# Kernel optimization log

Hardware: AMD Instinct MI355X
Metric: run time of the kernel (lower is better)

The kernel has to match this reference:

```python
import jax, jax.numpy as jnp
import numpy as np

NUM_WIRES = 18
NUM_LAYERS = 3
BATCH = 64
DIM = 2 ** NUM_WIRES


def _apply_ry(psi, theta, w):
    # RY(t) = [[cos(t/2), -sin(t/2)], [sin(t/2), cos(t/2)]] on wire w (wire 0 = MSB)
    B = psi.shape[0]
    c = jnp.cos(theta * 0.5).astype(psi.dtype)
    s = jnp.sin(theta * 0.5).astype(psi.dtype)
    p = psi.reshape(B, 2 ** w, 2, -1)
    a, b = p[:, :, 0], p[:, :, 1]
    return jnp.stack([c * a - s * b, s * a + c * b], axis=2).reshape(B, -1)


def _apply_rz(psi, theta, w):
    # RZ(t) = diag(e^{-i t/2}, e^{+i t/2}) on wire w
    B = psi.shape[0]
    half = (theta * 0.5).astype(jnp.complex64)
    p0 = jnp.exp(-1j * half)
    p1 = jnp.exp(1j * half)
    p = psi.reshape(B, 2 ** w, 2, -1)
    return jnp.stack([p0 * p[:, :, 0], p1 * p[:, :, 1]], axis=2).reshape(B, -1)


def _apply_cnot_adjacent(psi, w):
    # CNOT with control w, target w+1: flip target bit where control bit = 1
    B = psi.shape[0]
    p = psi.reshape(B, 2 ** w, 2, 2, -1)
    p = p.at[:, :, 1].set(p[:, :, 1, ::-1])
    return p.reshape(B, -1)


def _expval_z(psi, w):
    # <Z_w> = P(bit_w = 0) - P(bit_w = 1)
    B = psi.shape[0]
    prob = (psi.real ** 2 + psi.imag ** 2).reshape(B, 2 ** w, 2, -1)
    p = prob.sum(axis=(1, 3))  # (B, 2)
    return p[:, 0] - p[:, 1]


def _circuit(psi, params):
    for layer in range(params.shape[0]):
        for w in range(NUM_WIRES):
            psi = _apply_ry(psi, params[layer, 0, w], w)
            psi = _apply_rz(psi, params[layer, 1, w], w)
        for w in range(NUM_WIRES - 1):
            psi = _apply_cnot_adjacent(psi, w)
    # expvals of PauliZ on every wire -> (B, num_wires)
    return jnp.stack([_expval_z(psi, w) for w in range(NUM_WIRES)], axis=-1)


def setup_inputs() -> dict:
    key = jax.random.key(0)
    k1, k2, k3, k4, k5 = jax.random.split(key, 5)
    state_re = jax.random.normal(k1, (BATCH, DIM), dtype=jnp.float32)
    state_im = jax.random.normal(k2, (BATCH, DIM), dtype=jnp.float32)
    norm = jnp.sqrt(jnp.sum(state_re ** 2 + state_im ** 2, axis=-1, keepdims=True))
    state_re = state_re / norm
    state_im = state_im / norm
    params = jax.random.normal(k3, (NUM_LAYERS, 2, NUM_WIRES), dtype=jnp.float32)
    head_w = jax.random.normal(k4, (1, NUM_WIRES), dtype=jnp.float32) / np.sqrt(NUM_WIRES)
    head_b = jax.random.normal(k5, (1,), dtype=jnp.float32) / np.sqrt(NUM_WIRES)
    return {"state_re": state_re, "state_im": state_im, "params": params,
            "head_w": head_w, "head_b": head_b}


def reference(state_re, state_im, params, head_w, head_b):
    psi = (state_re + 1j * state_im).astype(jnp.complex64)  # (B, 2^n)
    feats = _circuit(psi, params)                            # (B, n)
    out = feats @ head_w.T + head_b                          # (B, 1)
    return out[:, 0]
```

## Files before the change

### kernel.cpp

```cpp
#include <hip/hip_runtime.h>


#define LROW 36u
#define LDSW 2304u

static __device__ __forceinline__ float rfl(float x) {
    return __int_as_float(__builtin_amdgcn_readfirstlane(__float_as_int(x)));
}

static __device__ __forceinline__ void unpack2(unsigned u, float& re, float& im) {
    re = __uint_as_float(u << 16);
    im = __uint_as_float(u & 0xFFFF0000u);
}
static __device__ __forceinline__ unsigned packbf(float a, float b) {
    unsigned ua = __float_as_uint(a); ua += 0x7FFFu + ((ua >> 16) & 1u);
    unsigned ub = __float_as_uint(b); ub += 0x7FFFu + ((ub >> 16) & 1u);
    return (ua >> 16) | (ub & 0xFFFF0000u);
}

static __device__ __forceinline__ void sq_pair(float& a0r, float& a0i, float& a1r, float& a1i,
                                               float c, float s, float pc, float ps) {
    const float t0r = fmaf(c, a0r, -(s * a1r));
    const float t0i = fmaf(c, a0i, -(s * a1i));
    const float t1r = fmaf(s, a0r,  c * a1r);
    const float t1i = fmaf(s, a0i,  c * a1i);
    a0r = t0r; a0i = t0i;
    a1r = fmaf(pc, t1r, -(ps * t1i));
    a1i = fmaf(pc, t1i,  (ps * t1r));
}

template<int J>
__device__ __forceinline__ void sqg(float* ar, float* ai, float c, float s, float pc, float ps) {
#pragma unroll
    for (int r = 0; r < 32; ++r) {
        if (((r >> J) & 1) == 0) {
            const int r1 = r + (1 << J);
            sq_pair(ar[r], ai[r], ar[r1], ai[r1], c, s, pc, ps);
        }
    }
}

struct BCoef { float C[7], S[7], PC[7], PS[7]; };

static __device__ __forceinline__ void passB_body(float* ar, float* ai, float* Lb,
                                                  const BCoef& k, int l) {
    const int L0 = l & 1;
    sqg<4>(ar, ai, k.C[4], k.S[4], k.PC[4], k.PS[4]);
    sqg<3>(ar, ai, k.C[3], k.S[3], k.PC[3], k.PS[3]);
    sqg<2>(ar, ai, k.C[2], k.S[2], k.PC[2], k.PS[2]);

    const unsigned tb = (unsigned)L0 * 144u + (unsigned)(l >> 1);
#pragma unroll
    for (int g = 0; g < 8; ++g)
#pragma unroll
        for (int c = 0; c < 4; ++c)
            Lb[tb + g * 288 + c * 36] = ar[4*g+c];
#pragma unroll
    for (int q = 0; q < 8; ++q) {
        const float4 v = *(const float4*)&Lb[(unsigned)l * LROW + (q << 2)];
        ar[4*q+0] = v.x; ar[4*q+1] = v.y; ar[4*q+2] = v.z; ar[4*q+3] = v.w;
    }
#pragma unroll
    for (int g = 0; g < 8; ++g)
#pragma unroll
        for (int c = 0; c < 4; ++c)
            Lb[tb + g * 288 + c * 36] = ai[4*g+c];
#pragma unroll
    for (int q = 0; q < 8; ++q) {
        const float4 v = *(const float4*)&Lb[(unsigned)l * LROW + (q << 2)];
        ai[4*q+0] = v.x; ai[4*q+1] = v.y; ai[4*q+2] = v.z; ai[4*q+3] = v.w;
    }

    sqg<4>(ar, ai, k.C[6], k.S[6], k.PC[6], k.PS[6]);
    sqg<3>(ar, ai, k.C[5], k.S[5], k.PC[5], k.PS[5]);
    sqg<2>(ar, ai, k.C[1], k.S[1], k.PC[1], k.PS[1]);
    sqg<1>(ar, ai, k.C[0], k.S[0], k.PC[0], k.PS[0]);

#pragma unroll
    for (int q = 0; q < 8; ++q)
        *(float4*)&Lb[(unsigned)l * LROW + (q << 2)] =
            make_float4(ar[4*q+0], ar[4*q+1], ar[4*q+2], ar[4*q+3]);
#pragma unroll
    for (int g = 0; g < 8; ++g)
#pragma unroll
        for (int c = 0; c < 4; ++c)
            ar[4*g+c] = Lb[tb + g * 288 + c * 36];
#pragma unroll
    for (int q = 0; q < 8; ++q)
        *(float4*)&Lb[(unsigned)l * LROW + (q << 2)] =
            make_float4(ai[4*q+0], ai[4*q+1], ai[4*q+2], ai[4*q+3]);
#pragma unroll
    for (int g = 0; g < 8; ++g)
#pragma unroll
        for (int c = 0; c < 4; ++c)
            ai[4*g+c] = Lb[tb + g * 288 + c * 36];
}

static __device__ __forceinline__ void passB_coefs(BCoef& k, const float* pl) {
#pragma unroll
    for (int j = 0; j < 7; ++j) {
        const int w = 6 - j;
        float sv, cv;
        __sincosf(0.5f * pl[w], &sv, &cv);  k.S[j] = rfl(sv);  k.C[j] = rfl(cv);
        __sincosf(pl[18 + w], &sv, &cv);    k.PS[j] = rfl(sv); k.PC[j] = rfl(cv);
    }
}

__global__ __launch_bounds__(128) void passB1_k(const float* re, const float* im,
                                                unsigned* u, const float* __restrict__ params)
{
    __shared__ float lds[2 * LDSW];
    const int t   = threadIdx.x;
    const int l   = t & 63;
    const int wib = t >> 6;
    float* Lb = lds + wib * LDSW;
    const int wv  = ((int)blockIdx.x << 1) | wib;
    const int b   = wv >> 7;
    const int mid = wv & 127;
    const int L5 = (l >> 5) & 1, L4 = (l >> 4) & 1, L3 = (l >> 3) & 1, L2 = (l >> 2) & 1;
    const int L1 = (l >> 1) & 1, L0 = l & 1;

    const unsigned base = ((unsigned)b << 18) | ((unsigned)mid << 4);
    const unsigned sel  = (L5 << 17) | (L4 << 16) | (L3 << 12) | (L2 << 11) | (L1 << 3) | (L0 << 2);

    float ar[32], ai[32];
#pragma unroll
    for (int g = 0; g < 8; ++g) {
        const unsigned n = base + sel + ((unsigned)g << 13);
        const float4 vr = *(const float4*)&re[n];
        const float4 vi = *(const float4*)&im[n];
        ar[4*g+0] = vr.x; ar[4*g+1] = vr.y; ar[4*g+2] = vr.z; ar[4*g+3] = vr.w;
        ai[4*g+0] = vi.x; ai[4*g+1] = vi.y; ai[4*g+2] = vi.z; ai[4*g+3] = vi.w;
    }

    BCoef k; passB_coefs(k, params);
    passB_body(ar, ai, Lb, k, l);

#pragma unroll
    for (int g = 0; g < 8; ++g) {
        const int h = (L5 << 6) | (L4 << 5) | (g << 2) | (L3 << 1) | L2;
        const unsigned n = base + ((unsigned)h << 11) + (L1 << 3) + (L0 << 2);
        uint4 pv;
        pv.x = packbf(ar[4*g+0], ai[4*g+0]);
        pv.y = packbf(ar[4*g+1], ai[4*g+1]);
        pv.z = packbf(ar[4*g+2], ai[4*g+2]);
        pv.w = packbf(ar[4*g+3], ai[4*g+3]);
        *(uint4*)&u[n] = pv;
    }
}

__global__ __launch_bounds__(128) void passBk_k(const unsigned* __restrict__ src,
                                                unsigned* __restrict__ dst,
                                                const float* __restrict__ params, int layer)
{
    __shared__ float lds[2 * LDSW];
    const int t   = threadIdx.x;
    const int l   = t & 63;
    const int wib = t >> 6;
    float* Lb = lds + wib * LDSW;
    const int wv  = ((int)blockIdx.x << 1) | wib;
    const int b   = wv >> 7;
    const int mid = wv & 127;
    const int L5 = (l >> 5) & 1, L4 = (l >> 4) & 1, L3 = (l >> 3) & 1, L2 = (l >> 2) & 1;
    const int L1 = (l >> 1) & 1, L0 = l & 1;

    const unsigned base = ((unsigned)b << 18) | ((unsigned)mid << 4);
    const unsigned sel  = (L5 << 17) | (L4 << 16) | (L3 << 12) | (L2 << 11) | (L1 << 3) | (L0 << 2);

    float ar[32], ai[32];
#pragma unroll
    for (int g = 0; g < 8; ++g) {
        const unsigned n = base + sel + ((unsigned)g << 13);
        const uint4 pv = *(const uint4*)&src[n];
        unpack2(pv.x, ar[4*g+0], ai[4*g+0]);
        unpack2(pv.y, ar[4*g+1], ai[4*g+1]);
        unpack2(pv.z, ar[4*g+2], ai[4*g+2]);
        unpack2(pv.w, ar[4*g+3], ai[4*g+3]);
    }

    BCoef k; passB_coefs(k, params + layer * 36);
    passB_body(ar, ai, Lb, k, l);

#pragma unroll
    for (int g = 0; g < 8; ++g) {
        int h = (L5 << 6) | (L4 << 5) | (g << 2) | (L3 << 1) | L2;
        int x = h ^ (h >> 1); x ^= x >> 2; x ^= x >> 4;
        const unsigned n = base + ((unsigned)x << 11) + (L1 << 3) + (L0 << 2);
        uint4 pv;
        pv.x = packbf(ar[4*g+0], ai[4*g+0]);
        pv.y = packbf(ar[4*g+1], ai[4*g+1]);
        pv.z = packbf(ar[4*g+2], ai[4*g+2]);
        pv.w = packbf(ar[4*g+3], ai[4*g+3]);
        *(uint4*)&dst[n] = pv;
    }
}

template<bool FIRST, bool FINAL>
__global__ __launch_bounds__(128) void passA_k(const unsigned* __restrict__ src,
                                               unsigned* __restrict__ dst,
                                               const float* __restrict__ params, int layer,
                                               const float* __restrict__ hw,
                                               const float* __restrict__ hb,
                                               float* __restrict__ out)
{
    __shared__ float lds[2 * LDSW];
    const int t   = threadIdx.x;
    const int l   = t & 63;
    const int wib = t >> 6;
    float* Lb = lds + wib * LDSW;
    const int wv  = ((int)blockIdx.x << 1) | wib;
    const int b   = wv >> 7;
    const int L   = wv & 127;
    const int hip = FIRST ? (L ^ (L >> 1)) : L;
    const int n11 = L & 1;
    const unsigned baseL = ((unsigned)b << 18) | ((unsigned)hip << 11);
    const unsigned baseS = ((unsigned)b << 18) | ((unsigned)L << 11);

    uint4 U[8];
#pragma unroll
    for (int g = 0; g < 8; ++g)
        U[g] = *(const uint4*)&src[baseL + ((unsigned)g << 8) + ((unsigned)l << 2)];

    float C[11], S[11], PC[11], PS[11];
    const float* pl = params + layer * 36;
#pragma unroll
    for (int p = 0; p < 11; ++p) {
        const int w = 17 - p;
        float sv, cv;
        __sincosf(0.5f * pl[w], &sv, &cv);  S[p] = rfl(sv);  C[p] = rfl(cv);
        __sincosf(pl[18 + w], &sv, &cv);    PS[p] = rfl(sv); PC[p] = rfl(cv);
    }

    float ar[32], ai[32];
#pragma unroll
    for (int g = 0; g < 8; ++g) {
        unpack2(U[g].x, ar[4*g+0], ai[4*g+0]);
        unpack2(U[g].y, ar[4*g+1], ai[4*g+1]);
        unpack2(U[g].z, ar[4*g+2], ai[4*g+2]);
        unpack2(U[g].w, ar[4*g+3], ai[4*g+3]);
        sq_pair(ar[4*g+0], ai[4*g+0], ar[4*g+2], ai[4*g+2], C[1], S[1], PC[1], PS[1]);
        sq_pair(ar[4*g+1], ai[4*g+1], ar[4*g+3], ai[4*g+3], C[1], S[1], PC[1], PS[1]);
        sq_pair(ar[4*g+0], ai[4*g+0], ar[4*g+1], ai[4*g+1], C[0], S[0], PC[0], PS[0]);
        sq_pair(ar[4*g+2], ai[4*g+2], ar[4*g+3], ai[4*g+3], C[0], S[0], PC[0], PS[0]);
    }

    sqg<4>(ar, ai, C[10], S[10], PC[10], PS[10]);
    sqg<3>(ar, ai, C[9],  S[9],  PC[9],  PS[9]);
    sqg<2>(ar, ai, C[8],  S[8],  PC[8],  PS[8]);

    {
        const int side   = (l >> 5) & 1;
        const float c7   = C[7];
        const float bco  = side ? S[7] : -S[7];
        const float qc   = side ? PC[7] : 1.f;
        const float qs   = side ? PS[7] : 0.f;
#pragma unroll
        for (int r = 0; r < 32; ++r) {
            const float pr = __shfl_xor(ar[r], 32);
            const float pi = __shfl_xor(ai[r], 32);
            const float tr = fmaf(c7, ar[r], bco * pr);
            const float ti = fmaf(c7, ai[r], bco * pi);
            ar[r] = fmaf(qc, tr, -(qs * ti));
            ai[r] = fmaf(qc, ti,  (qs * tr));
        }
    }

    const unsigned tb = (unsigned)((l >> 5) & 1) * 144u + (unsigned)(l & 31);
#pragma unroll
    for (int g = 0; g < 8; ++g)
#pragma unroll
        for (int c = 0; c < 4; ++c)
            Lb[tb + g * 288 + c * 36] = ar[4*g+c];
#pragma unroll
    for (int q = 0; q < 8; ++q) {
        const float4 v = *(const float4*)&Lb[(unsigned)l * LROW + (q << 2)];
        ar[4*q+0] = v.x; ar[4*q+1] = v.y; ar[4*q+2] = v.z; ar[4*q+3] = v.w;
    }
#pragma unroll
    for (int g = 0; g < 8; ++g)
#pragma unroll
        for (int c = 0; c < 4; ++c)
            Lb[tb + g * 288 + c * 36] = ai[4*g+c];
#pragma unroll
    for (int q = 0; q < 8; ++q) {
        const float4 v = *(const float4*)&Lb[(unsigned)l * LROW + (q << 2)];
        ai[4*q+0] = v.x; ai[4*q+1] = v.y; ai[4*q+2] = v.z; ai[4*q+3] = v.w;
    }

    sqg<4>(ar, ai, C[6], S[6], PC[6], PS[6]);
    sqg<3>(ar, ai, C[5], S[5], PC[5], PS[5]);
    sqg<2>(ar, ai, C[4], S[4], PC[4], PS[4]);
    sqg<1>(ar, ai, C[3], S[3], PC[3], PS[3]);
    sqg<0>(ar, ai, C[2], S[2], PC[2], PS[2]);

#pragma unroll
    for (int q = 0; q < 8; ++q)
        *(float4*)&Lb[(unsigned)l * LROW + (q << 2)] =
            make_float4(ar[4*q+0], ar[4*q+1], ar[4*q+2], ar[4*q+3]);
#pragma unroll
    for (int g = 0; g < 8; ++g)
#pragma unroll
        for (int c = 0; c < 4; ++c)
            ar[4*g+c] = Lb[tb + g * 288 + c * 36];
#pragma unroll
    for (int q = 0; q < 8; ++q)
        *(float4*)&Lb[(unsigned)l * LROW + (q << 2)] =
            make_float4(ai[4*q+0], ai[4*q+1], ai[4*q+2], ai[4*q+3]);
#pragma unroll
    for (int g = 0; g < 8; ++g)
#pragma unroll
        for (int c = 0; c < 4; ++c)
            ai[4*g+c] = Lb[tb + g * 288 + c * 36];

    const int msk = n11 ? 0x1FF : 0;

    if (!FINAL) {
#pragma unroll
        for (int g = 0; g < 8; ++g) {
            int h = (g << 6) | l;
            int x = h ^ (h >> 1); x ^= x >> 2; x ^= x >> 4; x ^= x >> 8;
            x ^= msk;
            const int y = x & 1;
            const float r0 = ar[4*g+0], r1 = ar[4*g+1], r2 = ar[4*g+2], r3 = ar[4*g+3];
            const float i0 = ai[4*g+0], i1 = ai[4*g+1], i2 = ai[4*g+2], i3 = ai[4*g+3];
            uint4 pv;
            pv.x = y ? packbf(r2, i2) : packbf(r0, i0);
            pv.y = y ? packbf(r3, i3) : packbf(r1, i1);
            pv.z = y ? packbf(r1, i1) : packbf(r3, i3);
            pv.w = y ? packbf(r0, i0) : packbf(r2, i2);
            *(uint4*)&dst[baseS + ((unsigned)x << 2)] = pv;
        }
    } else {
        float Ghi = 0.f;
#pragma unroll
        for (int j = 0; j < 7; ++j) {
            const float wv_ = hw[6 - j];
            Ghi += ((L >> j) & 1) ? -wv_ : wv_;
        }
        float acc = 0.f;
#pragma unroll
        for (int g = 0; g < 8; ++g) {
            int h = (g << 6) | l;
            int x = h ^ (h >> 1); x ^= x >> 2; x ^= x >> 4; x ^= x >> 8;
            x ^= msk;
            const float q0 = fmaf(ar[4*g+0], ar[4*g+0], ai[4*g+0] * ai[4*g+0]);
            const float q1 = fmaf(ar[4*g+1], ar[4*g+1], ai[4*g+1] * ai[4*g+1]);
            const float q2 = fmaf(ar[4*g+2], ar[4*g+2], ai[4*g+2] * ai[4*g+2]);
            const float q3 = fmaf(ar[4*g+3], ar[4*g+3], ai[4*g+3] * ai[4*g+3]);
            const float psum = (q0 + q1) + (q2 + q3);
            const float d1   = (q0 + q1) - (q2 + q3);
            const float d0   = (q0 - q1) - (q2 - q3);
            float Gm = 0.f;
#pragma unroll
            for (int j = 0; j < 9; ++j) {
                const float wv_ = hw[15 - j];
                Gm += ((x >> j) & 1) ? -wv_ : wv_;
            }
            const float ys = (x & 1) ? -1.f : 1.f;
            acc += psum * (Ghi + Gm) + ys * fmaf(d1, hw[16], d0 * hw[17]);
        }
        if (L == 0 && l == 0) acc += hb[0];
#pragma unroll
        for (int off = 32; off > 0; off >>= 1) acc += __shfl_xor(acc, off);
        if (l == 0) atomicAdd(&out[b], acc);
    }
}

extern "C" void kernel_launch(void* const* d_in, const int* in_sizes, int n_in,
                              void* d_out, int out_size, void* d_ws, size_t ws_size,
                              hipStream_t stream)
{
    const float* re0    = (const float*)d_in[0];
    const float* im0    = (const float*)d_in[1];
    unsigned* u0        = (unsigned*)d_in[0];
    unsigned* u1        = (unsigned*)d_in[1];
    const float* params = (const float*)d_in[2];
    const float* hw     = (const float*)d_in[3];
    const float* hb     = (const float*)d_in[4];
    float* out          = (float*)d_out;
    (void)in_sizes; (void)n_in; (void)d_ws; (void)ws_size;

    hipMemsetAsync(out, 0, (size_t)out_size * sizeof(float), stream);

    const dim3 grid(4096), blk(128);
    passB1_k             <<<grid, blk, 0, stream>>>(re0, im0, u0, params);
    passA_k<true,  false><<<grid, blk, 0, stream>>>(u0, u1, params, 0, nullptr, nullptr, nullptr);
    passBk_k             <<<grid, blk, 0, stream>>>(u1, u0, params, 1);
    passA_k<false, false><<<grid, blk, 0, stream>>>(u0, u1, params, 1, nullptr, nullptr, nullptr);
    passBk_k             <<<grid, blk, 0, stream>>>(u1, u0, params, 2);
    passA_k<false, true ><<<grid, blk, 0, stream>>>(u0, nullptr, params, 2, hw, hb, out);
}
```

Before: 394.8 us.

## Use packed f32x2 complex math and pack to bf16 before final LDS transpose

Stores each amplitude as an interleaved (re,im) f32x2 and rewrites the RY+RZ pair update with inline v_pk_mul_f32/v_pk_fma_f32 instructions, cutting VALU instruction count roughly in half. The second LDS transpose now packs values to bf16 first, so one uint transpose replaces two float transposes before the global store. The final-layer path keeps the float transposes. Risks: inline asm with SGPR operands constrains the scheduler, and the interleaved layout may change register allocation and occupancy.

Measured after the change: 372.6 us, median of 3. 5.6% less time.

```diff
diff --git a/kernel.cpp b/kernel.cpp
--- a/kernel.cpp
+++ b/kernel.cpp
@@ -4,106 +4,117 @@
 #define LROW 36u
 #define LDSW 2304u
 
+typedef float f32x2 __attribute__((ext_vector_type(2)));
+
 static __device__ __forceinline__ float rfl(float x) {
     return __int_as_float(__builtin_amdgcn_readfirstlane(__float_as_int(x)));
 }
 
-static __device__ __forceinline__ void unpack2(unsigned u, float& re, float& im) {
-    re = __uint_as_float(u << 16);
-    im = __uint_as_float(u & 0xFFFF0000u);
-}
-static __device__ __forceinline__ unsigned packbf(float a, float b) {
-    unsigned ua = __float_as_uint(a); ua += 0x7FFFu + ((ua >> 16) & 1u);
-    unsigned ub = __float_as_uint(b); ub += 0x7FFFu + ((ub >> 16) & 1u);
+static __device__ __forceinline__ f32x2 unpk(unsigned u) {
+    f32x2 v;
+    v.x = __uint_as_float(u << 16);
+    v.y = __uint_as_float(u & 0xFFFF0000u);
+    return v;
+}
+
+static __device__ __forceinline__ unsigned packbf(f32x2 a) {
+    unsigned ua = __float_as_uint(a.x); ua += 0x7FFFu + ((ua >> 16) & 1u);
+    unsigned ub = __float_as_uint(a.y); ub += 0x7FFFu + ((ub >> 16) & 1u);
     return (ua >> 16) | (ub & 0xFFFF0000u);
 }
 
-static __device__ __forceinline__ void sq_pair(float& a0r, float& a0i, float& a1r, float& a1i,
-                                               float c, float s, float pc, float ps) {
-    const float t0r = fmaf(c, a0r, -(s * a1r));
-    const float t0i = fmaf(c, a0i, -(s * a1i));
-    const float t1r = fmaf(s, a0r,  c * a1r);
-    const float t1i = fmaf(s, a0i,  c * a1i);
-    a0r = t0r; a0i = t0i;
-    a1r = fmaf(pc, t1r, -(ps * t1i));
-    a1i = fmaf(pc, t1i,  (ps * t1r));
+static __device__ __forceinline__ void sq_pair2(f32x2& a0, f32x2& a1,
+                                                f32x2 ry, f32x2 pz) {
+    f32x2 m, n, t1, p;
+    asm("v_pk_mul_f32 %0, %1, %2 op_sel:[1,0] op_sel_hi:[1,1]"
+        : "=v"(m) : "s"(ry), "v"(a1));
+    asm("v_pk_mul_f32 %0, %1, %2 op_sel:[0,0] op_sel_hi:[0,1]"
+        : "=v"(n) : "s"(ry), "v"(a1));
+    asm("v_pk_fma_f32 %0, %1, %2, %3 op_sel:[1,0,0] op_sel_hi:[1,1,1]"
+        : "=v"(t1) : "s"(ry), "v"(a0), "v"(n));
+    asm("v_pk_fma_f32 %0, %1, %0, %2 op_sel:[0,0,0] op_sel_hi:[0,1,1] neg_lo:[0,0,1] neg_hi:[0,0,1]"
+        : "+v"(a0) : "s"(ry), "v"(m));
+    asm("v_pk_mul_f32 %0, %1, %2 op_sel:[1,1] op_sel_hi:[1,0]"
+        : "=v"(p) : "s"(pz), "v"(t1));
+    asm("v_pk_fma_f32 %0, %1, %2, %3 op_sel:[0,0,0] op_sel_hi:[0,1,1] neg_lo:[0,0,1] neg_hi:[0,0,0]"
+        : "=v"(a1) : "s"(pz), "v"(t1), "v"(p));
 }
 
 template<int J>
-__device__ __forceinline__ void sqg(float* ar, float* ai, float c, float s, float pc, float ps) {
+__device__ __forceinline__ void sqg2(f32x2* a, f32x2 ry, f32x2 pz) {
 #pragma unroll
     for (int r = 0; r < 32; ++r) {
         if (((r >> J) & 1) == 0) {
-            const int r1 = r + (1 << J);
-            sq_pair(ar[r], ai[r], ar[r1], ai[r1], c, s, pc, ps);
-        }
-    }
-}
-
-struct BCoef { float C[7], S[7], PC[7], PS[7]; };
-
-static __device__ __forceinline__ void passB_body(float* ar, float* ai, float* Lb,
-                                                  const BCoef& k, int l) {
-    const int L0 = l & 1;
-    sqg<4>(ar, ai, k.C[4], k.S[4], k.PC[4], k.PS[4]);
-    sqg<3>(ar, ai, k.C[3], k.S[3], k.PC[3], k.PS[3]);
-    sqg<2>(ar, ai, k.C[2], k.S[2], k.PC[2], k.PS[2]);
-
-    const unsigned tb = (unsigned)L0 * 144u + (unsigned)(l >> 1);
+            sq_pair2(a[r], a[r + (1 << J)], ry, pz);
+        }
+    }
+}
+
+static __device__ __forceinline__ void t1_float(f32x2* a, float* Lb, int l, unsigned tb) {
 #pragma unroll
     for (int g = 0; g < 8; ++g)
 #pragma unroll
         for (int c = 0; c < 4; ++c)
-            Lb[tb + g * 288 + c * 36] = ar[4*g+c];
+            Lb[tb + g * 288 + c * 36] = a[4*g+c].x;
 #pragma unroll
     for (int q = 0; q < 8; ++q) {
         const float4 v = *(const float4*)&Lb[(unsigned)l * LROW + (q << 2)];
-        ar[4*q+0] = v.x; ar[4*q+1] = v.y; ar[4*q+2] = v.z; ar[4*q+3] = v.w;
+        a[4*q+0].x = v.x; a[4*q+1].x = v.y; a[4*q+2].x = v.z; a[4*q+3].x = v.w;
     }
 #pragma unroll
     for (int g = 0; g < 8; ++g)
 #pragma unroll
         for (int c = 0; c < 4; ++c)
-            Lb[tb + g * 288 + c * 36] = ai[4*g+c];
+            Lb[tb + g * 288 + c * 36] = a[4*g+c].y;
 #pragma unroll
     for (int q = 0; q < 8; ++q) {
         const float4 v = *(const float4*)&Lb[(unsigned)l * LROW + (q << 2)];
-        ai[4*q+0] = v.x; ai[4*q+1] = v.y; ai[4*q+2] = v.z; ai[4*q+3] = v.w;
-    }
-
-    sqg<4>(ar, ai, k.C[6], k.S[6], k.PC[6], k.PS[6]);
-    sqg<3>(ar, ai, k.C[5], k.S[5], k.PC[5], k.PS[5]);
-    sqg<2>(ar, ai, k.C[1], k.S[1], k.PC[1], k.PS[1]);
-    sqg<1>(ar, ai, k.C[0], k.S[0], k.PC[0], k.PS[0]);
-
-#pragma unroll
-    for (int q = 0; q < 8; ++q)
-        *(float4*)&Lb[(unsigned)l * LROW + (q << 2)] =
-            make_float4(ar[4*q+0], ar[4*q+1], ar[4*q+2], ar[4*q+3]);
+        a[4*q+0].y = v.x; a[4*q+1].y = v.y; a[4*q+2].y = v.z; a[4*q+3].y = v.w;
+    }
+}
+
+static __device__ __forceinline__ void pack_t2(f32x2* a, float* Lb, int l, unsigned tb,
+                                               unsigned v[8][4]) {
+    unsigned* Lu = (unsigned*)Lb;
+#pragma unroll
+    for (int q = 0; q < 8; ++q) {
+        uint4 pv;
+        pv.x = packbf(a[4*q+0]); pv.y = packbf(a[4*q+1]);
+        pv.z = packbf(a[4*q+2]); pv.w = packbf(a[4*q+3]);
+        *(uint4*)&Lu[(unsigned)l * LROW + (q << 2)] = pv;
+    }
 #pragma unroll
     for (int g = 0; g < 8; ++g)
 #pragma unroll
         for (int c = 0; c < 4; ++c)
-            ar[4*g+c] = Lb[tb + g * 288 + c * 36];
-#pragma unroll
-    for (int q = 0; q < 8; ++q)
-        *(float4*)&Lb[(unsigned)l * LROW + (q << 2)] =
-            make_float4(ai[4*q+0], ai[4*q+1], ai[4*q+2], ai[4*q+3]);
-#pragma unroll
-    for (int g = 0; g < 8; ++g)
-#pragma unroll
-        for (int c = 0; c < 4; ++c)
-            ai[4*g+c] = Lb[tb + g * 288 + c * 36];
-}
-
-static __device__ __forceinline__ void passB_coefs(BCoef& k, const float* pl) {
+            v[g][c] = Lu[tb + g * 288 + c * 36];
+}
+
+struct BCoef2 { f32x2 RY[7], PZ[7]; };
+
+static __device__ __forceinline__ void passB_coefs(BCoef2& k, const float* pl) {
 #pragma unroll
     for (int j = 0; j < 7; ++j) {
         const int w = 6 - j;
         float sv, cv;
-        __sincosf(0.5f * pl[w], &sv, &cv);  k.S[j] = rfl(sv);  k.C[j] = rfl(cv);
-        __sincosf(pl[18 + w], &sv, &cv);    k.PS[j] = rfl(sv); k.PC[j] = rfl(cv);
-    }
+        __sincosf(0.5f * pl[w], &sv, &cv);
+        k.RY[j].x = rfl(cv); k.RY[j].y = rfl(sv);
+        __sincosf(pl[18 + w], &sv, &cv);
+        k.PZ[j].x = rfl(cv); k.PZ[j].y = rfl(sv);
+    }
+}
+
+static __device__ __forceinline__ void passB_body(f32x2* a, float* Lb,
+                                                  const BCoef2& k, int l) {
+    const unsigned tb = (unsigned)(l & 1) * 144u + (unsigned)(l >> 1);
+    sqg2<4>(a, k.RY[4], k.PZ[4]);
+    sqg2<3>(a, k.RY[3], k.PZ[3]);
+    sqg2<2>(a, k.RY[2], k.PZ[2]);
+    t1_float(a, Lb, l, tb);
+    sqg2<4>(a, k.RY[6], k.PZ[6]);
+    sqg2<3>(a, k.RY[5], k.PZ[5]);
+    sqg2<2>(a, k.RY[1], k.PZ[1]);
+    sqg2<1>(a, k.RY[0], k.PZ[0]);
 }
 
 __global__ __launch_bounds__(128) void passB1_k(const float* re, const float* im,
@@ -123,29 +134,29 @@
     const unsigned base = ((unsigned)b << 18) | ((unsigned)mid << 4);
     const unsigned sel  = (L5 << 17) | (L4 << 16) | (L3 << 12) | (L2 << 11) | (L1 << 3) | (L0 << 2);
 
-    float ar[32], ai[32];
+    f32x2 a[32];
 #pragma unroll
     for (int g = 0; g < 8; ++g) {
         const unsigned n = base + sel + ((unsigned)g << 13);
         const float4 vr = *(const float4*)&re[n];
         const float4 vi = *(const float4*)&im[n];
-        ar[4*g+0] = vr.x; ar[4*g+1] = vr.y; ar[4*g+2] = vr.z; ar[4*g+3] = vr.w;
-        ai[4*g+0] = vi.x; ai[4*g+1] = vi.y; ai[4*g+2] = vi.z; ai[4*g+3] = vi.w;
-    }
-
-    BCoef k; passB_coefs(k, params);
-    passB_body(ar, ai, Lb, k, l);
+        a[4*g+0].x = vr.x; a[4*g+0].y = vi.x;
+        a[4*g+1].x = vr.y; a[4*g+1].y = vi.y;
+        a[4*g+2].x = vr.z; a[4*g+2].y = vi.z;
+        a[4*g+3].x = vr.w; a[4*g+3].y = vi.w;
+    }
+
+    BCoef2 k; passB_coefs(k, params);
+    passB_body(a, Lb, k, l);
+
+    unsigned v[8][4];
+    pack_t2(a, Lb, l, (unsigned)L0 * 144u + (unsigned)(l >> 1), v);
 
 #pragma unroll
     for (int g = 0; g < 8; ++g) {
         const int h = (L5 << 6) | (L4 << 5) | (g << 2) | (L3 << 1) | L2;
         const unsigned n = base + ((unsigned)h << 11) + (L1 << 3) + (L0 << 2);
-        uint4 pv;
-        pv.x = packbf(ar[4*g+0], ai[4*g+0]);
-        pv.y = packbf(ar[4*g+1], ai[4*g+1]);
-        pv.z = packbf(ar[4*g+2], ai[4*g+2]);
-        pv.w = packbf(ar[4*g+3], ai[4*g+3]);
-        *(uint4*)&u[n] = pv;
+        *(uint4*)&u[n] = make_uint4(v[g][0], v[g][1], v[g][2], v[g][3]);
     }
 }
 
@@ -167,31 +178,29 @@
     const unsigned base = ((unsigned)b << 18) | ((unsigned)mid << 4);
     const unsigned sel  = (L5 << 17) | (L4 << 16) | (L3 << 12) | (L2 << 11) | (L1 << 3) | (L0 << 2);
 
-    float ar[32], ai[32];
+    f32x2 a[32];
 #pragma unroll
     for (int g = 0; g < 8; ++g) {
         const unsigned n = base + sel + ((unsigned)g << 13);
         const uint4 pv = *(const uint4*)&src[n];
-        unpack2(pv.x, ar[4*g+0], ai[4*g+0]);
-        unpack2(pv.y, ar[4*g+1], ai[4*g+1]);
-        unpack2(pv.z, ar[4*g+2], ai[4*g+2]);
-        unpack2(pv.w, ar[4*g+3], ai[4*g+3]);
-    }
-
-    BCoef k; passB_coefs(k, params + layer * 36);
-    passB_body(ar, ai, Lb, k, l);
+        a[4*g+0] = unpk(pv.x);
+        a[4*g+1] = unpk(pv.y);
+        a[4*g+2] = unpk(pv.z);
+        a[4*g+3] = unpk(pv.w);
+    }
+
+    BCoef2 k; passB_coefs(k, params + layer * 36);
+    passB_body(a, Lb, k, l);
+
+    unsigned v[8][4];
+    pack_t2(a, Lb, l, (unsigned)L0 * 144u + (unsigned)(l >> 1), v);
 
 #pragma unroll
     for (int g = 0; g < 8; ++g) {
         int h = (L5 << 6) | (L4 << 5) | (g << 2) | (L3 << 1) | L2;
         int x = h ^ (h >> 1); x ^= x >> 2; x ^= x >> 4;
         const unsigned n = base + ((unsigned)x << 11) + (L1 << 3) + (L0 << 2);
-        uint4 pv;
-        pv.x = packbf(ar[4*g+0], ai[4*g+0]);
-        pv.y = packbf(ar[4*g+1], ai[4*g+1]);
-        pv.z = packbf(ar[4*g+2], ai[4*g+2]);
-        pv.w = packbf(ar[4*g+3], ai[4*g+3]);
-        *(uint4*)&dst[n] = pv;
+        *(uint4*)&dst[n] = make_uint4(v[g][0], v[g][1], v[g][2], v[g][3]);
     }
 }
 
@@ -221,116 +230,99 @@
     for (int g = 0; g < 8; ++g)
         U[g] = *(const uint4*)&src[baseL + ((unsigned)g << 8) + ((unsigned)l << 2)];
 
-    float C[11], S[11], PC[11], PS[11];
+    f32x2 RY2[11], PZ2[11];
     const float* pl = params + layer * 36;
 #pragma unroll
     for (int p = 0; p < 11; ++p) {
         const int w = 17 - p;
         float sv, cv;
-        __sincosf(0.5f * pl[w], &sv, &cv);  S[p] = rfl(sv);  C[p] = rfl(cv);
-        __sincosf(pl[18 + w], &sv, &cv);    PS[p] = rfl(sv); PC[p] = rfl(cv);
-    }
-
-    float ar[32], ai[32];
-#pragma unroll
-    for (int g = 0; g < 8; ++g) {
-        unpack2(U[g].x, ar[4*g+0], ai[4*g+0]);
-        unpack2(U[g].y, ar[4*g+1], ai[4*g+1]);
-        unpack2(U[g].z, ar[4*g+2], ai[4*g+2]);
-        unpack2(U[g].w, ar[4*g+3], ai[4*g+3]);
-        sq_pair(ar[4*g+0], ai[4*g+0], ar[4*g+2], ai[4*g+2], C[1], S[1], PC[1], PS[1]);
-        sq_pair(ar[4*g+1], ai[4*g+1], ar[4*g+3], ai[4*g+3], C[1], S[1], PC[1], PS[1]);
-        sq_pair(ar[4*g+0], ai[4*g+0], ar[4*g+1], ai[4*g+1], C[0], S[0], PC[0], PS[0]);
-        sq_pair(ar[4*g+2], ai[4*g+2], ar[4*g+3], ai[4*g+3], C[0], S[0], PC[0], PS[0]);
-    }
-
-    sqg<4>(ar, ai, C[10], S[10], PC[10], PS[10]);
-    sqg<3>(ar, ai, C[9],  S[9],  PC[9],  PS[9]);
-    sqg<2>(ar, ai, C[8],  S[8],  PC[8],  PS[8]);
+        __sincosf(0.5f * pl[w], &sv, &cv);
+        RY2[p].x = rfl(cv); RY2[p].y = rfl(sv);
+        __sincosf(pl[18 + w], &sv, &cv);
+        PZ2[p].x = rfl(cv); PZ2[p].y = rfl(sv);
+    }
+
+    f32x2 a[32];
+#pragma unroll
+    for (int g = 0; g < 8; ++g) {
+        a[4*g+0] = unpk(U[g].x);
+        a[4*g+1] = unpk(U[g].y);
+        a[4*g+2] = unpk(U[g].z);
+        a[4*g+3] = unpk(U[g].w);
+        sq_pair2(a[4*g+0], a[4*g+2], RY2[1], PZ2[1]);
+        sq_pair2(a[4*g+1], a[4*g+3], RY2[1], PZ2[1]);
+        sq_pair2(a[4*g+0], a[4*g+1], RY2[0], PZ2[0]);
+        sq_pair2(a[4*g+2], a[4*g+3], RY2[0], PZ2[0]);
+    }
+
+    sqg2<4>(a, RY2[10], PZ2[10]);
+    sqg2<3>(a, RY2[9],  PZ2[9]);
+    sqg2<2>(a, RY2[8],  PZ2[8]);
 
     {
         const int side   = (l >> 5) & 1;
-        const float c7   = C[7];
-        const float bco  = side ? S[7] : -S[7];
-        const float qc   = side ? PC[7] : 1.f;
-        const float qs   = side ? PS[7] : 0.f;
+        const float c7   = RY2[7].x;
+        const float bco  = side ? RY2[7].y : -RY2[7].y;
+        const float qc   = side ? PZ2[7].x : 1.f;
+        const float qs   = side ? PZ2[7].y : 0.f;
 #pragma unroll
         for (int r = 0; r < 32; ++r) {
-            const float pr = __shfl_xor(ar[r], 32);
-            const float pi = __shfl_xor(ai[r], 32);
-            const float tr = fmaf(c7, ar[r], bco * pr);
-            const float ti = fmaf(c7, ai[r], bco * pi);
-            ar[r] = fmaf(qc, tr, -(qs * ti));
-            ai[r] = fmaf(qc, ti,  (qs * tr));
+            const float pr = __shfl_xor(a[r].x, 32);
+            const float pi = __shfl_xor(a[r].y, 32);
+            const float tr = fmaf(c7, a[r].x, bco * pr);
+            const float ti = fmaf(c7, a[r].y, bco * pi);
+            a[r].x = fmaf(qc, tr, -(qs * ti));
+            a[r].y = fmaf(qc, ti,  (qs * tr));
         }
     }
 
     const unsigned tb = (unsigned)((l >> 5) & 1) * 144u + (unsigned)(l & 31);
-#pragma unroll
-    for (int g = 0; g < 8; ++g)
-#pragma unroll
-        for (int c = 0; c < 4; ++c)
-            Lb[tb + g * 288 + c * 36] = ar[4*g+c];
-#pragma unroll
-    for (int q = 0; q < 8; ++q) {
-        const float4 v = *(const float4*)&Lb[(unsigned)l * LROW + (q << 2)];
-        ar[4*q+0] = v.x; ar[4*q+1] = v.y; ar[4*q+2] = v.z; ar[4*q+3] = v.w;
-    }
-#pragma unroll
-    for (int g = 0; g < 8; ++g)
-#pragma unroll
-        for (int c = 0; c < 4; ++c)
-            Lb[tb + g * 288 + c * 36] = ai[4*g+c];
-#pragma unroll
-    for (int q = 0; q < 8; ++q) {
-        const float4 v = *(const float4*)&Lb[(unsigned)l * LROW + (q << 2)];
-        ai[4*q+0] = v.x; ai[4*q+1] = v.y; ai[4*q+2] = v.z; ai[4*q+3] = v.w;
-    }
-
-    sqg<4>(ar, ai, C[6], S[6], PC[6], PS[6]);
-    sqg<3>(ar, ai, C[5], S[5], PC[5], PS[5]);
-    sqg<2>(ar, ai, C[4], S[4], PC[4], PS[4]);
-    sqg<1>(ar, ai, C[3], S[3], PC[3], PS[3]);
-    sqg<0>(ar, ai, C[2], S[2], PC[2], PS[2]);
-
-#pragma unroll
-    for (int q = 0; q < 8; ++q)
-        *(float4*)&Lb[(unsigned)l * LROW + (q << 2)] =
-            make_float4(ar[4*q+0], ar[4*q+1], ar[4*q+2], ar[4*q+3]);
-#pragma unroll
-    for (int g = 0; g < 8; ++g)
-#pragma unroll
-        for (int c = 0; c < 4; ++c)
-            ar[4*g+c] = Lb[tb + g * 288 + c * 36];
-#pragma unroll
-    for (int q = 0; q < 8; ++q)
-        *(float4*)&Lb[(unsigned)l * LROW + (q << 2)] =
-            make_float4(ai[4*q+0], ai[4*q+1], ai[4*q+2], ai[4*q+3]);
-#pragma unroll
-    for (int g = 0; g < 8; ++g)
-#pragma unroll
-        for (int c = 0; c < 4; ++c)
-            ai[4*g+c] = Lb[tb + g * 288 + c * 36];
+    t1_float(a, Lb, l, tb);
+
+    sqg2<4>(a, RY2[6], PZ2[6]);
+    sqg2<3>(a, RY2[5], PZ2[5]);
+    sqg2<2>(a, RY2[4], PZ2[4]);
+    sqg2<1>(a, RY2[3], PZ2[3]);
+    sqg2<0>(a, RY2[2], PZ2[2]);
 
     const int msk = n11 ? 0x1FF : 0;
 
     if (!FINAL) {
+        unsigned v[8][4];
+        pack_t2(a, Lb, l, tb, v);
 #pragma unroll
         for (int g = 0; g < 8; ++g) {
             int h = (g << 6) | l;
             int x = h ^ (h >> 1); x ^= x >> 2; x ^= x >> 4; x ^= x >> 8;
             x ^= msk;
             const int y = x & 1;
-            const float r0 = ar[4*g+0], r1 = ar[4*g+1], r2 = ar[4*g+2], r3 = ar[4*g+3];
-            const float i0 = ai[4*g+0], i1 = ai[4*g+1], i2 = ai[4*g+2], i3 = ai[4*g+3];
             uint4 pv;
-            pv.x = y ? packbf(r2, i2) : packbf(r0, i0);
-            pv.y = y ? packbf(r3, i3) : packbf(r1, i1);
-            pv.z = y ? packbf(r1, i1) : packbf(r3, i3);
-            pv.w = y ? packbf(r0, i0) : packbf(r2, i2);
+            pv.x = y ? v[g][2] : v[g][0];
+            pv.y = y ? v[g][3] : v[g][1];
+            pv.z = y ? v[g][1] : v[g][3];
+            pv.w = y ? v[g][0] : v[g][2];
             *(uint4*)&dst[baseS + ((unsigned)x << 2)] = pv;
         }
     } else {
+#pragma unroll
+        for (int q = 0; q < 8; ++q)
+            *(float4*)&Lb[(unsigned)l * LROW + (q << 2)] =
+                make_float4(a[4*q+0].x, a[4*q+1].x, a[4*q+2].x, a[4*q+3].x);
+#pragma unroll
+        for (int g = 0; g < 8; ++g)
+#pragma unroll
+            for (int c = 0; c < 4; ++c)
+                a[4*g+c].x = Lb[tb + g * 288 + c * 36];
+#pragma unroll
+        for (int q = 0; q < 8; ++q)
+            *(float4*)&Lb[(unsigned)l * LROW + (q << 2)] =
+                make_float4(a[4*q+0].y, a[4*q+1].y, a[4*q+2].y, a[4*q+3].y);
+#pragma unroll
+        for (int g = 0; g < 8; ++g)
+#pragma unroll
+            for (int c = 0; c < 4; ++c)
+                a[4*g+c].y = Lb[tb + g * 288 + c * 36];
+
         float Ghi = 0.f;
 #pragma unroll
         for (int j = 0; j < 7; ++j) {
@@ -343,10 +335,10 @@
             int h = (g << 6) | l;
             int x = h ^ (h >> 1); x ^= x >> 2; x ^= x >> 4; x ^= x >> 8;
             x ^= msk;
-            const float q0 = fmaf(ar[4*g+0], ar[4*g+0], ai[4*g+0] * ai[4*g+0]);
-            const float q1 = fmaf(ar[4*g+1], ar[4*g+1], ai[4*g+1] * ai[4*g+1]);
-            const float q2 = fmaf(ar[4*g+2], ar[4*g+2], ai[4*g+2] * ai[4*g+2]);
-            const float q3 = fmaf(ar[4*g+3], ar[4*g+3], ai[4*g+3] * ai[4*g+3]);
+            const float q0 = fmaf(a[4*g+0].x, a[4*g+0].x, a[4*g+0].y * a[4*g+0].y);
+            const float q1 = fmaf(a[4*g+1].x, a[4*g+1].x, a[4*g+1].y * a[4*g+1].y);
+            const float q2 = fmaf(a[4*g+2].x, a[4*g+2].x, a[4*g+2].y * a[4*g+2].y);
+            const float q3 = fmaf(a[4*g+3].x, a[4*g+3].x, a[4*g+3].y * a[4*g+3].y);
             const float psum = (q0 + q1) + (q2 + q3);
             const float d1   = (q0 + q1) - (q2 + q3);
             const float d0   = (q0 - q1) - (q2 - q3);
```
